# Kernel optimization log

Measured on AMD Instinct MI355X. Metric: run time of the kernel, lower is better.

## Reference

```python
import jax, jax.numpy as jnp
import numpy as np

NUM_HEADS = 16

def _feat(x):
    # tanh feature map mapped to (0,1): (tanh(x)+1)/2
    return (jnp.tanh(x) + 1.0) * 0.5

def setup_inputs() -> dict:
    key = jax.random.key(0)
    k1, k2, k3 = jax.random.split(key, 3)
    B, S, D = 4, 4096, 1024
    q = jax.random.normal(k1, (B, S, D), dtype=jnp.float32)
    k = jax.random.normal(k2, (B, S, D), dtype=jnp.float32)
    v = jax.random.normal(k3, (B, S, D), dtype=jnp.float32)
    return {"q": q, "k": k, "v": v}

def reference(q, k, v):
    B, S, D = q.shape
    H = NUM_HEADS
    d = D // H
    qh = _feat(q.reshape(B, S, H, d))          # (B,S,H,d)
    kh = _feat(k.reshape(B, S, H, d))          # (B,S,H,d)
    vh = v.reshape(B, S, H, d)                 # (B,S,H,e)
    # global kv summary: sum over sequence of outer products k_d v_e per head
    kv = jnp.einsum('bshd,bshe->bdeh', kh, vh)            # (B,d,e,H)
    k_reduced = jnp.sum(kh, axis=1) + 1e-8                # (B,H,d)
    z = 1.0 / jnp.einsum('bshd,bhd->bsh', qh, k_reduced)  # (B,S,H)
    out = jnp.einsum('bshd,bdeh,bsh->bshe', qh, kv, z)    # (B,S,H,e)
    return out.reshape(B, S, H * d)
```

## Files before the change

### kernel.cpp

```cpp
#include <hip/hip_runtime.h>
#include <hip/hip_fp16.h>

#define B_ 4
#define S_ 4096
#define H_ 16
#define D_ 1024
#define HD_ 64
#define NC_ 16

typedef __fp16 hf8 __attribute__((ext_vector_type(8)));
typedef _Float16 h2 __attribute__((ext_vector_type(2)));
typedef float f32x4 __attribute__((ext_vector_type(4)));

__device__ __forceinline__ float featmap(float x) {
  float e = __expf(-2.0f * x);
  return __builtin_amdgcn_rcpf(1.0f + e);
}

__device__ __forceinline__ unsigned pk2u(float a, float b) {
  auto r = __builtin_amdgcn_cvt_pkrtz(a, b);
  unsigned u;
  __builtin_memcpy(&u, &r, 4);
  return u;
}

__device__ __forceinline__ float dot2acc(h2 a, h2 b, float c) {
#if __has_builtin(__builtin_amdgcn_fdot2)
  return __builtin_amdgcn_fdot2(a, b, c, false);
#else
  return c + (float)a[0] * (float)b[0] + (float)a[1] * (float)b[1];
#endif
}

__global__ __launch_bounds__(256, 4) void mh_p1(
    const float* __restrict__ kg, const float* __restrict__ vg,
    float* __restrict__ kvp, float* __restrict__ kredp) {
  __shared__ __align__(16) char khT[8192];
  __shared__ __align__(16) char vT[8192];
  __shared__ float ksp[256][4];

  const int bid = blockIdx.x;
  const int bh = bid & 63, c = bid >> 6;
  const int b = bh >> 4, h = bh & 15;
  const int t = threadIdx.x, w = t >> 6, l = t & 63;

  const size_t rowbase = (size_t)b * S_ * D_ + (size_t)h * HD_;
  const float* kb = kg + rowbase;
  const float* vb = vg + rowbase;
  const int s0 = c * 256;

  f32x4 acc[4];
#pragma unroll
  for (int et = 0; et < 4; ++et) acc[et] = (f32x4){0.f, 0.f, 0.f, 0.f};
  float ksacc[4] = {0.f, 0.f, 0.f, 0.f};

  const int rq = (t >> 4) * 4;
  const int cq = (t & 15) * 4;
  const int swzW = ((t & 15) & 7) << 4;
  const int wroff = (rq * 2) ^ swzW;

  const int arow = l & 15;
  const int kgB = (l >> 4) * 16;

#pragma unroll 1
  for (int tile = 0; tile < 4; ++tile) {
    const float* kr = kb + (size_t)(s0 + tile * 64 + rq) * D_ + cq;
    const float* vr = vb + (size_t)(s0 + tile * 64 + rq) * D_ + cq;
    float4 kv0 = *(const float4*)kr;
    float4 kv1 = *(const float4*)(kr + D_);
    float4 kv2 = *(const float4*)(kr + 2 * D_);
    float4 kv3 = *(const float4*)(kr + 3 * D_);
    float4 vv0 = *(const float4*)vr;
    float4 vv1 = *(const float4*)(vr + D_);
    float4 vv2 = *(const float4*)(vr + 2 * D_);
    float4 vv3 = *(const float4*)(vr + 3 * D_);
    const float fk[4][4] = {
        {featmap(kv0.x), featmap(kv0.y), featmap(kv0.z), featmap(kv0.w)},
        {featmap(kv1.x), featmap(kv1.y), featmap(kv1.z), featmap(kv1.w)},
        {featmap(kv2.x), featmap(kv2.y), featmap(kv2.z), featmap(kv2.w)},
        {featmap(kv3.x), featmap(kv3.y), featmap(kv3.z), featmap(kv3.w)}};
    const float fv[4][4] = {{vv0.x, vv0.y, vv0.z, vv0.w},
                            {vv1.x, vv1.y, vv1.z, vv1.w},
                            {vv2.x, vv2.y, vv2.z, vv2.w},
                            {vv3.x, vv3.y, vv3.z, vv3.w}};
#pragma unroll
    for (int j = 0; j < 4; ++j) {
      ksacc[j] += fk[0][j] + fk[1][j] + fk[2][j] + fk[3][j];
      uint2 ku = {pk2u(fk[0][j], fk[1][j]), pk2u(fk[2][j], fk[3][j])};
      uint2 vu = {pk2u(fv[0][j], fv[1][j]), pk2u(fv[2][j], fv[3][j])};
      *(uint2*)&khT[(cq + j) * 128 + wroff] = ku;
      *(uint2*)&vT [(cq + j) * 128 + wroff] = vu;
    }
    __syncthreads();
#pragma unroll
    for (int kk = 0; kk < 2; ++kk) {
      const int sbyte = kk * 64 + kgB;
      hf8 af;
      {
        const int d = w * 16 + arow;
        float4 tmp = *(const float4*)&khT[d * 128 + (sbyte ^ (((d >> 2) & 7) << 4))];
        __builtin_memcpy(&af, &tmp, 16);
      }
#pragma unroll
      for (int et = 0; et < 4; ++et) {
        const int e = et * 16 + arow;
        hf8 bf;
        float4 tmp = *(const float4*)&vT[e * 128 + (sbyte ^ (((e >> 2) & 7) << 4))];
        __builtin_memcpy(&bf, &tmp, 16);
        acc[et] = __builtin_amdgcn_mfma_f32_16x16x32_f16(af, bf, acc[et], 0, 0, 0);
      }
    }
    __syncthreads();
  }

  {
    float* dst = kvp + ((size_t)(c * 64 + bh)) * 4096;
    const int col = l & 15, rg4 = (l >> 4) * 4;
#pragma unroll
    for (int et = 0; et < 4; ++et)
#pragma unroll
      for (int r = 0; r < 4; ++r)
        dst[(w * 16 + rg4 + r) * 64 + et * 16 + col] = acc[et][r];
  }
#pragma unroll
  for (int j = 0; j < 4; ++j) ksp[t][j] = ksacc[j];
  __syncthreads();
  if (t < 64) {
    float s = 0.f;
#pragma unroll
    for (int g = 0; g < 16; ++g) s += ksp[(t >> 2) + 16 * g][t & 3];
    kredp[(size_t)(c * 64 + bh) * 64 + t] = s;
  }
}

__global__ __launch_bounds__(256) void mh_p15(
    const float* __restrict__ kvp, const float* __restrict__ kredp,
    float* __restrict__ kv, float* __restrict__ kred) {
  const int i = blockIdx.x * 256 + threadIdx.x;
  float s = 0.f;
#pragma unroll
  for (int c = 0; c < NC_; ++c) s += kvp[(size_t)c * (64 * 4096) + i];
  kv[i] = s;
  if (i < 64 * 64) {
    float r = 0.f;
#pragma unroll
    for (int c = 0; c < NC_; ++c) r += kredp[c * 4096 + i];
    kred[i] = r + 1e-8f;
  }
}

__global__ __launch_bounds__(256, 3) void mh_p2(
    const float* __restrict__ qg, const float* __restrict__ kvg,
    const float* __restrict__ kredg, float* __restrict__ outg) {
  __shared__ __align__(16) char qt[32768];
  __shared__ __align__(16) char kvT[8192];
  __shared__ __align__(16) char kredh[128];

  const int bid = blockIdx.x;
  const int bh = bid >> 4, chunk = bid & 15;
  const int b = bh >> 4, h = bh & 15;
  const int blockrow = chunk * 256;
  const int t = threadIdx.x, w = t >> 6, l = t & 63;

  const int tr = t >> 4, tc = (t & 15) * 4;
  const int swst = (tr & 7) << 4;
#pragma unroll
  for (int i = 0; i < 16; ++i) {
    const int row = tr + i * 16;
    float4 qv = *(const float4*)&qg[((size_t)(b * S_) + blockrow + row) * D_ + h * HD_ + tc];
    uint2 u = {pk2u(featmap(qv.x), featmap(qv.y)),
               pk2u(featmap(qv.z), featmap(qv.w))};
    *(uint2*)&qt[row * 128 + ((tc * 2) ^ swst)] = u;
  }
#pragma unroll
  for (int i = 0; i < 16; ++i) {
    const int idx = i * 256 + t;
    const int kk = idx >> 6, e = idx & 63;
    *(__half*)&kvT[e * 128 + ((kk * 2) ^ ((e & 7) << 4))] =
        __float2half(kvg[(size_t)bh * 4096 + idx]);
  }
  if (t < 16) {
    float4 kr = *(const float4*)&kredg[bh * 64 + t * 4];
    uint2 u = {pk2u(kr.x, kr.y), pk2u(kr.z, kr.w)};
    *(uint2*)&kredh[t * 8] = u;
  }
  __syncthreads();

  const int col = l & 15;
  const int kB = (l >> 4) * 16;
  const int sw = (l & 7) << 4;

  f32x4 acc[4][4];
#pragma unroll
  for (int i = 0; i < 4; ++i)
#pragma unroll
    for (int j = 0; j < 4; ++j) acc[i][j] = (f32x4){0.f, 0.f, 0.f, 0.f};
  float zf[4];

  h2 kk0[4], kk1[4];
  {
    float4 r0 = *(const float4*)&kredh[kB];
    float4 r1 = *(const float4*)&kredh[64 + kB];
    __builtin_memcpy(kk0, &r0, 16);
    __builtin_memcpy(kk1, &r1, 16);
  }

#pragma unroll
  for (int rt = 0; rt < 4; ++rt) {
    const int row = w * 64 + rt * 16 + col;
    float4 a0r = *(const float4*)&qt[row * 128 + (kB ^ sw)];
    float4 a1r = *(const float4*)&qt[row * 128 + ((64 + kB) ^ sw)];
    hf8 af0, af1;
    __builtin_memcpy(&af0, &a0r, 16);
    __builtin_memcpy(&af1, &a1r, 16);
    h2 aa0[4], aa1[4];
    __builtin_memcpy(aa0, &a0r, 16);
    __builtin_memcpy(aa1, &a1r, 16);
    float zp = 0.f;
#pragma unroll
    for (int j = 0; j < 4; ++j) {
      zp = dot2acc(aa0[j], kk0[j], zp);
      zp = dot2acc(aa1[j], kk1[j], zp);
    }
    zp += __shfl_xor(zp, 16);
    zp += __shfl_xor(zp, 32);
    zf[rt] = __builtin_amdgcn_rcpf(zp);
#pragma unroll
    for (int et = 0; et < 4; ++et) {
      const int er = et * 16 + col;
      float4 b0r = *(const float4*)&kvT[er * 128 + (kB ^ sw)];
      float4 b1r = *(const float4*)&kvT[er * 128 + ((64 + kB) ^ sw)];
      hf8 bf0, bf1;
      __builtin_memcpy(&bf0, &b0r, 16);
      __builtin_memcpy(&bf1, &b1r, 16);
      acc[rt][et] = __builtin_amdgcn_mfma_f32_16x16x32_f16(af0, bf0, acc[rt][et], 0, 0, 0);
      acc[rt][et] = __builtin_amdgcn_mfma_f32_16x16x32_f16(af1, bf1, acc[rt][et], 0, 0, 0);
    }
  }

  const int rg4 = (l >> 4) * 4;
#pragma unroll
  for (int rt = 0; rt < 4; ++rt) {
#pragma unroll
    for (int r = 0; r < 4; ++r) {
      const float zr = __shfl(zf[rt], rg4 + r);
      const int grow = blockrow + w * 64 + rt * 16 + rg4 + r;
      float* op = &outg[((size_t)(b * S_) + grow) * D_ + h * HD_];
#pragma unroll
      for (int et = 0; et < 4; ++et)
        op[et * 16 + col] = acc[rt][et][r] * zr;
    }
  }
}

extern "C" void kernel_launch(void* const* d_in, const int* in_sizes, int n_in,
                              void* d_out, int out_size, void* d_ws, size_t ws_size,
                              hipStream_t stream) {
  const float* q = (const float*)d_in[0];
  const float* k = (const float*)d_in[1];
  const float* v = (const float*)d_in[2];
  float* out = (float*)d_out;
  float* ws = (float*)d_ws;

  float* kv    = ws;
  float* kred  = ws + 262144;
  float* kvp   = ws + 262144 + 4096;
  float* kredp = kvp + (size_t)NC_ * 262144;

  mh_p1 <<<64 * NC_, 256, 0, stream>>>(k, v, kvp, kredp);
  mh_p15<<<1024,     256, 0, stream>>>(kvp, kredp, kv, kred);
  mh_p2 <<<64 * 16,  256, 0, stream>>>(q, kv, kred, out);
}
```

Baseline: 63.51 us.

## Stage full 256-row K/V chunk in LDS before one MFMA pass

Phase 1 now loads and feature-maps all four 64-row tiles into a larger LDS buffer (32 KB each for K and V) with a new XOR swizzle, syncs once, then runs all MFMA steps. This removes the per-tile barrier pairs and lets all global loads be issued together, giving more memory-level parallelism. In exchange, LDS use per block rises to about 68 KB and launch bounds drop from 4 to 2 blocks per SM, which cuts occupancy.

```diff
diff --git a/kernel.cpp b/kernel.cpp
--- a/kernel.cpp
+++ b/kernel.cpp
@@ -32,11 +32,13 @@
 #endif
 }
 
-__global__ __launch_bounds__(256, 4) void mh_p1(
+__device__ __forceinline__ int swzf(int d) { return ((d ^ (d >> 2)) & 15) << 4; }
+
+__global__ __launch_bounds__(256, 2) void mh_p1(
     const float* __restrict__ kg, const float* __restrict__ vg,
     float* __restrict__ kvp, float* __restrict__ kredp) {
-  __shared__ __align__(16) char khT[8192];
-  __shared__ __align__(16) char vT[8192];
+  __shared__ __align__(16) char khT[32768];
+  __shared__ __align__(16) char vT[32768];
   __shared__ float ksp[256][4];
 
   const int bid = blockIdx.x;
@@ -49,23 +51,15 @@
   const float* vb = vg + rowbase;
   const int s0 = c * 256;
 
-  f32x4 acc[4];
-#pragma unroll
-  for (int et = 0; et < 4; ++et) acc[et] = (f32x4){0.f, 0.f, 0.f, 0.f};
+  const int cq = (t & 15) * 4;
+  const int sgrp = t >> 4;
   float ksacc[4] = {0.f, 0.f, 0.f, 0.f};
 
-  const int rq = (t >> 4) * 4;
-  const int cq = (t & 15) * 4;
-  const int swzW = ((t & 15) & 7) << 4;
-  const int wroff = (rq * 2) ^ swzW;
-
-  const int arow = l & 15;
-  const int kgB = (l >> 4) * 16;
-
-#pragma unroll 1
-  for (int tile = 0; tile < 4; ++tile) {
-    const float* kr = kb + (size_t)(s0 + tile * 64 + rq) * D_ + cq;
-    const float* vr = vb + (size_t)(s0 + tile * 64 + rq) * D_ + cq;
+#pragma unroll
+  for (int i = 0; i < 4; ++i) {
+    const int sq = sgrp * 4 + 64 * i;
+    const float* kr = kb + (size_t)(s0 + sq) * D_ + cq;
+    const float* vr = vb + (size_t)(s0 + sq) * D_ + cq;
     float4 kv0 = *(const float4*)kr;
     float4 kv1 = *(const float4*)(kr + D_);
     float4 kv2 = *(const float4*)(kr + 2 * D_);
@@ -83,34 +77,48 @@
                             {vv1.x, vv1.y, vv1.z, vv1.w},
                             {vv2.x, vv2.y, vv2.z, vv2.w},
                             {vv3.x, vv3.y, vv3.z, vv3.w}};
+    const int spos = sq * 2;
 #pragma unroll
     for (int j = 0; j < 4; ++j) {
+      const int d = cq + j;
+      const int off = spos ^ swzf(d);
       ksacc[j] += fk[0][j] + fk[1][j] + fk[2][j] + fk[3][j];
       uint2 ku = {pk2u(fk[0][j], fk[1][j]), pk2u(fk[2][j], fk[3][j])};
       uint2 vu = {pk2u(fv[0][j], fv[1][j]), pk2u(fv[2][j], fv[3][j])};
-      *(uint2*)&khT[(cq + j) * 128 + wroff] = ku;
-      *(uint2*)&vT [(cq + j) * 128 + wroff] = vu;
-    }
-    __syncthreads();
-#pragma unroll
-    for (int kk = 0; kk < 2; ++kk) {
-      const int sbyte = kk * 64 + kgB;
-      hf8 af;
-      {
-        const int d = w * 16 + arow;
-        float4 tmp = *(const float4*)&khT[d * 128 + (sbyte ^ (((d >> 2) & 7) << 4))];
-        __builtin_memcpy(&af, &tmp, 16);
-      }
-#pragma unroll
-      for (int et = 0; et < 4; ++et) {
-        const int e = et * 16 + arow;
-        hf8 bf;
-        float4 tmp = *(const float4*)&vT[e * 128 + (sbyte ^ (((e >> 2) & 7) << 4))];
-        __builtin_memcpy(&bf, &tmp, 16);
-        acc[et] = __builtin_amdgcn_mfma_f32_16x16x32_f16(af, bf, acc[et], 0, 0, 0);
-      }
-    }
-    __syncthreads();
+      *(uint2*)&khT[d * 512 + off] = ku;
+      *(uint2*)&vT [d * 512 + off] = vu;
+    }
+  }
+#pragma unroll
+  for (int j = 0; j < 4; ++j) ksp[t][j] = ksacc[j];
+  __syncthreads();
+
+  f32x4 acc[4];
+#pragma unroll
+  for (int et = 0; et < 4; ++et) acc[et] = (f32x4){0.f, 0.f, 0.f, 0.f};
+  const int arow = l & 15;
+  const int sub = (l >> 4) * 16;
+  const int dA = w * 16 + arow;
+  const int foA = swzf(dA);
+  int foB[4];
+#pragma unroll
+  for (int et = 0; et < 4; ++et) foB[et] = swzf(et * 16 + arow);
+
+#pragma unroll
+  for (int kk = 0; kk < 8; ++kk) {
+    const int sbyte = kk * 64 + sub;
+    hf8 af;
+    {
+      float4 tmp = *(const float4*)&khT[dA * 512 + (sbyte ^ foA)];
+      __builtin_memcpy(&af, &tmp, 16);
+    }
+#pragma unroll
+    for (int et = 0; et < 4; ++et) {
+      hf8 bf;
+      float4 tmp = *(const float4*)&vT[(et * 16 + arow) * 512 + (sbyte ^ foB[et])];
+      __builtin_memcpy(&bf, &tmp, 16);
+      acc[et] = __builtin_amdgcn_mfma_f32_16x16x32_f16(af, bf, acc[et], 0, 0, 0);
+    }
   }
 
   {
@@ -122,9 +130,6 @@
       for (int r = 0; r < 4; ++r)
         dst[(w * 16 + rg4 + r) * 64 + et * 16 + col] = acc[et][r];
   }
-#pragma unroll
-  for (int j = 0; j < 4; ++j) ksp[t][j] = ksacc[j];
-  __syncthreads();
   if (t < 64) {
     float s = 0.f;
 #pragma unroll
```

Result: no change. 63.11 us (-0.6%).
